# Kernel optimization log

Measured on AMD Instinct MI355X. Metric: run time of the kernel, lower is better.

The kernel has to match this reference:

```python
import jax, jax.numpy as jnp
import numpy as np

# EEACSF hyperparameters (module defaults)
CUTOFF = 5.2
ANG_CUTOFF = 3.5
RADIAL_ETA = 16.0
ANGULAR_ETA = 8.0
RDIV = 16          # radial_dist_divisions
ADIV = 4           # angular_dist_divisions
ZETA = 32.0
SECTIONS = 4       # angle_sections
R_START = 0.8
A_START = 0.8
N_SPECIES = 87     # size of periodic-table / valence table

N_ATOMS = 20000
N_EDGES = 640000       # radial edges
N_ANG_EDGES = 160000   # angular-graph edges
N_PAIRS = 560000       # angle pairs


def setup_inputs() -> dict:
    key = jax.random.key(0)
    ks = jax.random.split(key, 12)
    species = jax.random.randint(ks[0], (N_ATOMS,), 0, N_SPECIES)
    # radial graph: distances in (R_START, CUTOFF)
    distances = R_START + (CUTOFF - R_START) * jax.random.uniform(ks[1], (N_EDGES,), jnp.float32)
    switch = jax.random.uniform(ks[2], (N_EDGES,), jnp.float32)
    edge_src = jax.random.randint(ks[3], (N_EDGES,), 0, N_ATOMS)
    edge_dst = jax.random.randint(ks[4], (N_EDGES,), 0, N_ATOMS)
    # angular graph
    ang_angles = np.pi * jax.random.uniform(ks[5], (N_PAIRS,), jnp.float32)
    ang_distances = A_START + (ANG_CUTOFF - A_START) * jax.random.uniform(ks[6], (N_ANG_EDGES,), jnp.float32)
    ang_switch = jax.random.uniform(ks[7], (N_ANG_EDGES,), jnp.float32)
    ang_edge_dst = jax.random.randint(ks[8], (N_ANG_EDGES,), 0, N_ATOMS)
    angle_src = jax.random.randint(ks[9], (N_PAIRS,), 0, N_ANG_EDGES)
    angle_dst = jax.random.randint(ks[10], (N_PAIRS,), 0, N_ANG_EDGES)
    central_atom = jax.random.randint(ks[11], (N_PAIRS,), 0, N_ATOMS)
    # valence structure table (stands in for the preprocessed VALENCE_STRUCTURE constant)
    valence_table = jax.random.uniform(jax.random.fold_in(key, 99), (N_SPECIES, 4), jnp.float32)
    return {
        "species": species, "distances": distances, "switch": switch,
        "edge_src": edge_src, "edge_dst": edge_dst,
        "ang_angles": ang_angles, "ang_distances": ang_distances,
        "ang_switch": ang_switch, "ang_edge_dst": ang_edge_dst,
        "angle_src": angle_src, "angle_dst": angle_dst,
        "central_atom": central_atom, "valence_table": valence_table,
    }


def reference(species, distances, switch, edge_src, edge_dst,
              ang_angles, ang_distances, ang_switch, ang_edge_dst,
              angle_src, angle_dst, central_atom, valence_table):
    n_atoms = species.shape[0]
    valence = valence_table[species]                                  # [N,4]

    # ---- radial AEV ----
    shiftR = jnp.asarray(np.linspace(R_START, CUTOFF, RDIV + 1)[None, :-1], distances.dtype)
    x2 = RADIAL_ETA * (distances[:, None] - shiftR) ** 2              # [E,16]
    radial_terms = 0.25 * jnp.exp(-x2) * switch[:, None]              # [E,16]
    radial_aev = jax.ops.segment_sum(
        radial_terms[:, :, None] * valence[edge_dst, None, :],        # [E,16,4]
        edge_src, num_segments=n_atoms,
    ).reshape(n_atoms, -1)                                            # [N,64]

    # ---- angular AEV ----
    d12 = 0.5 * (ang_distances[angle_src] + ang_distances[angle_dst])[:, None]  # [P,1]
    angle_start = np.pi / (2 * SECTIONS)
    shiftZ = jnp.asarray((np.linspace(0, np.pi, SECTIONS + 1) + angle_start)[None, :-1], ang_distances.dtype)
    shiftA = jnp.asarray(np.linspace(A_START, ANG_CUTOFF, ADIV + 1)[None, :-1], ang_distances.dtype)
    factor1 = (0.5 + 0.5 * jnp.cos(ang_angles[:, None] - shiftZ)) ** ZETA       # [P,4]
    factor2 = jnp.exp(-ANGULAR_ETA * (d12 - shiftA) ** 2)                       # [P,4]
    angular_terms = (factor1[:, None, :] * factor2[:, :, None]).reshape(-1, SECTIONS * ADIV)
    angular_terms = angular_terms * 2 * (ang_switch[angle_src] * ang_switch[angle_dst])[:, None]  # [P,16]

    valence_dst = valence[ang_edge_dst]                               # [E2,4]
    vp = valence_dst[angle_src] + valence_dst[angle_dst]              # [P,4]
    vm = valence_dst[angle_src] * valence_dst[angle_dst]              # [P,4]
    valence_ang = (vp[:, :, None] * vm[:, None, :]).reshape(-1, 16)   # [P,16]

    angular_aev = jax.ops.segment_sum(
        angular_terms[:, :, None] * valence_ang[:, None, :],          # [P,16,16]
        central_atom, num_segments=n_atoms,
    ).reshape(n_atoms, -1)                                            # [N,256]

    onehot = jax.nn.one_hot(species, N_SPECIES, dtype=distances.dtype)  # [N,87]
    return jnp.concatenate((onehot, radial_aev, angular_aev), axis=-1)  # [N,407]
```

## Files before the change

### kernel.cpp

```cpp
#include <hip/hip_runtime.h>
#include <hip/hip_fp16.h>
#include <math.h>

#define NCOLS   407
#define RAD_OFF 87
#define ANG_OFF 151
#define T1      3072
#define KPT     (T1 / 256)
#define WB      32
#define MAXBKT  640
#define CAPF    1792
#define C2      (CAPF / 256)


typedef __attribute__((ext_vector_type(8))) _Float16 f16x8;
typedef __attribute__((ext_vector_type(4))) float    f32x4;

static __device__ inline unsigned pack2(float a, float b) {
    __half2 h = __floats2half2_rn(a, b);
    return *reinterpret_cast<unsigned*>(&h);
}
static __device__ inline float2 unpack2(unsigned u) {
    __half2 h = *reinterpret_cast<__half2*>(&u);
    return __half22float2(h);
}

__global__ __launch_bounds__(256) void zc_kernel(int* __restrict__ cursors) {
    int t = threadIdx.x;
    for (int i = t; i < 2 * MAXBKT; i += 256) cursors[i] = 0;
}

__global__ __launch_bounds__(256) void pass1_kernel(
    const float* __restrict__ dist, const float* __restrict__ sw,
    const int* __restrict__ esrc, const int* __restrict__ edst,
    const float* __restrict__ ang_angles,
    const float* __restrict__ ang_dist, const float* __restrict__ ang_sw,
    const int* __restrict__ ang_edge_dst,
    const int* __restrict__ psrc, const int* __restrict__ pdst,
    const int* __restrict__ central,
    const int* __restrict__ species, const float4* __restrict__ valence,
    uint4* __restrict__ edata,
    int* __restrict__ cur_rad, int* __restrict__ cur_ang,
    uint4* __restrict__ arr_rad, uint4* __restrict__ arr_ang,
    int n_edges, int n_pairs, int n_ang_edges,
    int nbkt, int nbe, int nt_rad)
{
    __shared__ uint4 buf[T1];
    __shared__ int   lh[MAXBKT];
    __shared__ int   gb[MAXBKT];
    __shared__ int   wtot[4];

    int bid = blockIdx.x;
    int t = threadIdx.x;

    if (bid < nbe) {
        int i = bid * 2560 + t;
        #pragma unroll
        for (int k = 0; k < 10; ++k, i += 256) {
            if (i < n_ang_edges) {
                float4 v = valence[species[ang_edge_dst[i]]];
                uint4 r;
                r.x = __float_as_uint(ang_dist[i]);
                r.y = __float_as_uint(ang_sw[i]);
                r.z = pack2(v.x, v.y);
                r.w = pack2(v.z, v.w);
                edata[i] = r;
            }
        }
        return;
    }

    int sbid = bid - nbe;
    int is_ang = sbid >= nt_rad;
    const int* key = is_ang ? central : esrc;
    int* cursor = is_ang ? cur_ang : cur_rad;
    int n   = is_ang ? n_pairs : n_edges;
    int off = (is_ang ? sbid - nt_rad : sbid) * T1;
    int cnt = min(T1, n - off);
    uint4* arr = is_ang ? arr_ang : arr_rad;

    for (int b = t; b < nbkt; b += 256) lh[b] = 0;
    __syncthreads();

    int meta[KPT];
    #pragma unroll
    for (int k = 0; k < KPT; ++k) {
        int i = off + k * 256 + t;
        meta[k] = -1;
        if (i < n) {
            int atom = key[i];
            int r = atomicAdd(&lh[atom >> 5], 1);
            meta[k] = (atom << 12) | r;
        }
    }
    __syncthreads();

    {
        int w = t >> 6, lane = t & 63;
        int W4  = (nbkt + 3) >> 2;
        int wlo = w * W4;
        int whi = min(wlo + W4, nbkt);
        int b0 = wlo + lane * 3;
        int c0 = (b0     < whi) ? lh[b0]     : 0;
        int c1 = (b0 + 1 < whi) ? lh[b0 + 1] : 0;
        int c2 = (b0 + 2 < whi) ? lh[b0 + 2] : 0;
        int lsum = c0 + c1 + c2;
        int s = lsum;
        #pragma unroll
        for (int o = 1; o < 64; o <<= 1) {
            int u = __shfl_up(s, o, 64);
            if (lane >= o) s += u;
        }
        int excl = s - lsum;
        if (c0) gb[b0]     = b0       * CAPF + atomicAdd(&cursor[b0],     c0);
        if (c1) gb[b0 + 1] = (b0 + 1) * CAPF + atomicAdd(&cursor[b0 + 1], c1);
        if (c2) gb[b0 + 2] = (b0 + 2) * CAPF + atomicAdd(&cursor[b0 + 2], c2);
        if (b0     < whi) lh[b0]     = excl;
        if (b0 + 1 < whi) lh[b0 + 1] = excl + c0;
        if (b0 + 2 < whi) lh[b0 + 2] = excl + c0 + c1;
        if (lane == 63) wtot[w] = s;
        __syncthreads();
        int wbase = 0;
        for (int ww = 0; ww < w; ++ww) wbase += wtot[ww];
        if (wbase) {
            if (b0     < whi) lh[b0]     += wbase;
            if (b0 + 1 < whi) lh[b0 + 1] += wbase;
            if (b0 + 2 < whi) lh[b0 + 2] += wbase;
        }
        __syncthreads();
    }

    #pragma unroll
    for (int k = 0; k < KPT; ++k) {
        if (meta[k] < 0) continue;
        int i = off + k * 256 + t;
        int atom = meta[k] >> 12, r = meta[k] & 4095;
        int b = atom >> 5;
        uint4 rec;
        if (!is_ang) {
            float d  = dist[i];
            float ps = 0.25f * sw[i];
            float4 v = valence[species[edst[i]]];
            rec.x = __float_as_uint(d);
            rec.y = pack2(ps * v.x, ps * v.y);
            rec.z = pack2(ps * v.z, ps * v.w);
            rec.w = (unsigned)atom;
        } else {
            rec.x = (unsigned)psrc[i];
            rec.y = (unsigned)pdst[i];
            rec.z = __float_as_uint(ang_angles[i]);
            rec.w = (unsigned)atom;
        }
        buf[lh[b] + r] = rec;
    }
    __syncthreads();

    #pragma unroll
    for (int k = 0; k < KPT; ++k) {
        int j = k * 256 + t;
        if (j < cnt) {
            uint4 r = buf[j];
            int b = (int)(r.w >> 5);
            int gpos = gb[b] + (j - lh[b]);
            if (gpos < (b + 1) * CAPF) arr[gpos] = r;
        }
    }
}

__global__ __launch_bounds__(256) void pass2B_kernel(
    const uint4* __restrict__ arr_rad, const uint4* __restrict__ arr_ang,
    const uint4* __restrict__ edata,
    const int* __restrict__ cur_rad, const int* __restrict__ cur_ang,
    const int* __restrict__ species,
    float* __restrict__ out, int nbkt, int n_atoms)
{
    __shared__ uint4 buf[CAPF];
    __shared__ unsigned short ord[CAPF];
    __shared__ int lh[WB];
    __shared__ int sA[WB + 1];
    __shared__ uint4 stg[4][256];

    int bid = blockIdx.x;
    int t = threadIdx.x;
    int g = bid >= nbkt;
    int b = g ? bid - nbkt : bid;
    int lo  = b * CAPF;
    int cnt = min(g ? cur_ang[b] : cur_rad[b], CAPF);
    const uint4* arr = g ? arr_ang : arr_rad;
    int loA = b << 5;

    if (t < WB) lh[t] = 0;
    __syncthreads();
    int myar[C2];
    #pragma unroll
    for (int c = 0; c < C2; ++c) {
        int j = c * 256 + t;
        myar[c] = -1;
        if (j < cnt) {
            uint4 r = arr[lo + j];
            buf[j] = r;
            int a = (int)r.w - loA;
            if ((unsigned)a < WB) {
                int rk = atomicAdd(&lh[a], 1);
                myar[c] = (a << 12) | rk;
            }
        }
    }
    __syncthreads();
    if (t < 64) {
        int v = (t < WB) ? lh[t] : 0;
        int s = v;
        #pragma unroll
        for (int o = 1; o < WB; o <<= 1) {
            int u = __shfl_up(s, o, 64);
            if (t >= o) s += u;
        }
        if (t < WB) sA[t + 1] = s;
        if (t == 0) sA[0] = 0;
    }
    __syncthreads();
    #pragma unroll
    for (int c = 0; c < C2; ++c) {
        if (myar[c] >= 0) {
            int j = c * 256 + t;
            ord[sA[myar[c] >> 12] + (myar[c] & 4095)] = (unsigned short)j;
        }
    }
    __syncthreads();

    int w    = t >> 6;
    int lane = t & 63;
    int m  = lane & 15;
    int g4 = lane >> 4;

    if (g) {
        const _Float16* hl = (const _Float16*)stg[w];
        int aw0 = w * 8;
        int R0 = sA[aw0], R1 = sA[aw0 + 8];
        int cur = aw0;
        f32x4 acc = {0.f, 0.f, 0.f, 0.f};

        for (int base = R0; base < R1; base += 64) {
            int idx = base + lane;
            unsigned q[16];
            if (idx < R1) {
                uint4 pr = buf[ord[idx]];
                int e1 = (int)pr.x;
                int e2 = (int)pr.y;
                float ang = __uint_as_float(pr.z);
                uint4 r1 = edata[e1];
                uint4 r2 = edata[e2];
                float d12 = 0.5f * (__uint_as_float(r1.x) + __uint_as_float(r2.x));
                float swp = 2.0f * __uint_as_float(r1.y) * __uint_as_float(r2.y);
                float2 v1a = unpack2(r1.z), v1b = unpack2(r1.w);
                float2 v2a = unpack2(r2.z), v2b = unpack2(r2.w);
                float vp[4] = {v1a.x + v2a.x, v1a.y + v2a.y, v1b.x + v2b.x, v1b.y + v2b.y};
                float vm[4] = {v1a.x * v2a.x, v1a.y * v2a.y, v1b.x * v2b.x, v1b.y * v2b.y};

                float sa, ca;
                __sincosf(ang, &sa, &ca);
                const float czv[4] = { 0.92387953f,  0.38268343f, -0.38268343f, -0.92387953f };
                const float szv[4] = { 0.38268343f,  0.92387953f,  0.92387953f,  0.38268343f };
                float f1v[4];
                #pragma unroll
                for (int z = 0; z < 4; ++z) {
                    float y = 0.5f + 0.5f * (ca * czv[z] + sa * szv[z]);
                    float y2 = y * y, y4 = y2 * y2, y8 = y4 * y4, y16 = y8 * y8;
                    f1v[z] = y16 * y16;
                }
                float f2sv[4];
                #pragma unroll
                for (int aa = 0; aa < 4; ++aa) {
                    float x = d12 - (0.8f + 0.675f * (float)aa);
                    f2sv[aa] = swp * __expf(-8.0f * x * x);
                }
                #pragma unroll
                for (int aa = 0; aa < 4; ++aa) {
                    q[aa * 2 + 0] = pack2(f2sv[aa] * f1v[0], f2sv[aa] * f1v[1]);
                    q[aa * 2 + 1] = pack2(f2sv[aa] * f1v[2], f2sv[aa] * f1v[3]);
                }
                #pragma unroll
                for (int i2 = 0; i2 < 4; ++i2) {
                    q[8 + i2 * 2 + 0] = pack2(vp[i2] * vm[0], vp[i2] * vm[1]);
                    q[8 + i2 * 2 + 1] = pack2(vp[i2] * vm[2], vp[i2] * vm[3]);
                }
            } else {
                #pragma unroll
                for (int k = 0; k < 16; ++k) q[k] = 0u;
            }
            stg[w][lane * 4 + 0] = make_uint4(q[0],  q[1],  q[2],  q[3]);
            stg[w][lane * 4 + 1] = make_uint4(q[4],  q[5],  q[6],  q[7]);
            stg[w][lane * 4 + 2] = make_uint4(q[8],  q[9],  q[10], q[11]);
            stg[w][lane * 4 + 3] = make_uint4(q[12], q[13], q[14], q[15]);
            asm volatile("s_waitcnt lgkmcnt(0)" ::: "memory");

            #pragma unroll
            for (int c = 0; c < 2; ++c) {
                int cbase = base + c * 32;
                if (cbase >= R1) break;
                while (cur < aw0 + 8) {
                    int abeg = sA[cur], aend = sA[cur + 1];
                    int lo_r = max(abeg, cbase) - cbase;
                    int hi_r = min(aend, cbase + 32) - cbase;
                    if (hi_r > lo_r) {
                        f16x8 wf, uf;
                        #pragma unroll
                        for (int i = 0; i < 8; ++i) {
                            int rr  = (g4 << 3) + i;
                            int row = c * 32 + rr;
                            bool live = (rr >= lo_r && rr < hi_r);
                            wf[i] = live ? hl[row * 32 + m] : (_Float16)0.0f;
                            uf[i] = hl[row * 32 + 16 + m];
                        }
                        acc = __builtin_amdgcn_mfma_f32_16x16x32_f16(wf, uf, acc, 0, 0, 0);
                    }
                    if (aend <= cbase + 32) {
                        int atom = loA + cur;
                        if (atom < n_atoms) {
                            float* orow = out + (size_t)atom * NCOLS + ANG_OFF;
                            #pragma unroll
                            for (int r = 0; r < 4; ++r)
                                orow[(g4 * 4 + r) * 16 + m] = acc[r];
                        }
                        acc = (f32x4){0.f, 0.f, 0.f, 0.f};
                        ++cur;
                    } else {
                        break;
                    }
                }
            }
            asm volatile("s_waitcnt lgkmcnt(0)" ::: "memory");
        }
        while (cur < aw0 + 8) {
            int atom = loA + cur;
            if (atom < n_atoms) {
                float* orow = out + (size_t)atom * NCOLS + ANG_OFF;
                #pragma unroll
                for (int r = 0; r < 4; ++r)
                    orow[(g4 * 4 + r) * 16 + m] = 0.0f;
            }
            ++cur;
        }
        return;
    }

    const _Float16* hl = (const _Float16*)buf;
    const float*    fl = (const float*)buf;
    float shiftm = 0.8f + 0.275f * (float)m;
    for (int ai = 0; ai < 8; ++ai) {
        int a = w * 8 + ai;
        int atom = loA + a;
        if (atom >= n_atoms) break;
        int beg = sA[a], end = sA[a + 1];
        f32x4 acc = {0.f, 0.f, 0.f, 0.f};

        for (int base = beg; base < end; base += 64) {
            int cnt2 = min(64, end - base);
            {
                f16x8 wf, uf;
                #pragma unroll
                for (int i = 0; i < 8; ++i) {
                    int k = (g4 << 3) + i;
                    int live = (k < cnt2);
                    int o = live ? (int)ord[base + k] : 0;
                    float d = fl[o * 4];
                    float x = d - shiftm;
                    float e = __expf(-16.0f * x * x);
                    wf[i] = live ? (_Float16)e : (_Float16)0.0f;
                    uf[i] = (live && m < 4) ? hl[o * 8 + 2 + m] : (_Float16)0.0f;
                }
                acc = __builtin_amdgcn_mfma_f32_16x16x32_f16(wf, uf, acc, 0, 0, 0);
            }
            if (cnt2 > 32) {
                f16x8 wf, uf;
                #pragma unroll
                for (int i = 0; i < 8; ++i) {
                    int k = 32 + (g4 << 3) + i;
                    int live = (k < cnt2);
                    int o = live ? (int)ord[base + k] : 0;
                    float d = fl[o * 4];
                    float x = d - shiftm;
                    float e = __expf(-16.0f * x * x);
                    wf[i] = live ? (_Float16)e : (_Float16)0.0f;
                    uf[i] = (live && m < 4) ? hl[o * 8 + 2 + m] : (_Float16)0.0f;
                }
                acc = __builtin_amdgcn_mfma_f32_16x16x32_f16(wf, uf, acc, 0, 0, 0);
            }
        }
        if (m < 4) {
            size_t rowbase = (size_t)atom * NCOLS;
            #pragma unroll
            for (int r = 0; r < 4; ++r)
                out[rowbase + RAD_OFF + (g4 * 4 + r) * 4 + m] = acc[r];
        }
    }

    for (int idx2 = t; idx2 < WB * 87; idx2 += 256) {
        int a = idx2 / 87, c = idx2 - a * 87;
        int atom = loA + a;
        if (atom < n_atoms)
            out[(size_t)atom * NCOLS + c] = (c == species[atom]) ? 1.0f : 0.0f;
    }
}

extern "C" void kernel_launch(void* const* d_in, const int* in_sizes, int n_in,
                              void* d_out, int out_size, void* d_ws, size_t ws_size,
                              hipStream_t stream) {
    const int*   species      = (const int*)  d_in[0];
    const float* distances    = (const float*)d_in[1];
    const float* switch_      = (const float*)d_in[2];
    const int*   edge_src     = (const int*)  d_in[3];
    const int*   edge_dst     = (const int*)  d_in[4];
    const float* ang_angles   = (const float*)d_in[5];
    const float* ang_dist     = (const float*)d_in[6];
    const float* ang_switch   = (const float*)d_in[7];
    const int*   ang_edge_dst = (const int*)  d_in[8];
    const int*   angle_src    = (const int*)  d_in[9];
    const int*   angle_dst    = (const int*)  d_in[10];
    const int*   central_atom = (const int*)  d_in[11];
    const float4* valence     = (const float4*)d_in[12];

    float* out = (float*)d_out;

    const int n_atoms     = in_sizes[0];
    const int n_edges     = in_sizes[1];
    const int n_ang_edges = in_sizes[6];
    const int n_pairs     = in_sizes[5];

    const int nbkt   = (n_atoms + WB - 1) / WB;
    const int nt_rad = (n_edges + T1 - 1) / T1;
    const int nt_ang = (n_pairs + T1 - 1) / T1;
    const int nbe    = (n_ang_edges + 2559) / 2560;

    char* ws = (char*)d_ws;
    size_t off = 0;
    auto alloc = [&](size_t bytes) -> void* {
        void* p = ws + off;
        off = (off + bytes + 15) & ~(size_t)15;
        return p;
    };
    uint4* arr_rad = (uint4*)alloc((size_t)nbkt * CAPF * 16);
    uint4* arr_ang = (uint4*)alloc((size_t)nbkt * CAPF * 16);
    uint4* edata   = (uint4*)alloc((size_t)n_ang_edges * 16);
    int*   cursors = (int*)  alloc((size_t)2 * MAXBKT * sizeof(int));
    int* cur_rad = cursors;
    int* cur_ang = cursors + MAXBKT;

    zc_kernel<<<1, 256, 0, stream>>>(cursors);

    pass1_kernel<<<nbe + nt_rad + nt_ang, 256, 0, stream>>>(
        distances, switch_, edge_src, edge_dst,
        ang_angles, ang_dist, ang_switch, ang_edge_dst,
        angle_src, angle_dst, central_atom,
        species, valence, edata,
        cur_rad, cur_ang, arr_rad, arr_ang,
        n_edges, n_pairs, n_ang_edges, nbkt, nbe, nt_rad);

    pass2B_kernel<<<2 * nbkt, 256, 0, stream>>>(
        arr_rad, arr_ang, edata, cur_rad, cur_ang, species, out, nbkt, n_atoms);
}
```

Measured before the change: 79.31 us.

## Replace atomic bucket cursors with deterministic two-pass tile histogram scan

Before, each pass1 tile reserved space in fixed-capacity bucket slots through global atomic cursors. Now a separate histogram pass counts keys per tile and bucket. A transposed scan plus a bucket-level scan then give exact, compact global offsets, and pass1 scatters into densely packed arrays with no atomics and no capacity clipping. This removes global atomic contention and the padded CAPF-sized arrays, but adds extra launches and a second read of the key arrays. The tile size is also shrunk.

```diff
diff --git a/kernel.cpp b/kernel.cpp
--- a/kernel.cpp
+++ b/kernel.cpp
@@ -5,7 +5,7 @@
 #define NCOLS   407
 #define RAD_OFF 87
 #define ANG_OFF 151
-#define T1      3072
+#define T1      2816
 #define KPT     (T1 / 256)
 #define WB      32
 #define MAXBKT  640
@@ -25,31 +25,17 @@
     return __half22float2(h);
 }
 
-__global__ __launch_bounds__(256) void zc_kernel(int* __restrict__ cursors) {
-    int t = threadIdx.x;
-    for (int i = t; i < 2 * MAXBKT; i += 256) cursors[i] = 0;
-}
-
-__global__ __launch_bounds__(256) void pass1_kernel(
-    const float* __restrict__ dist, const float* __restrict__ sw,
-    const int* __restrict__ esrc, const int* __restrict__ edst,
-    const float* __restrict__ ang_angles,
-    const float* __restrict__ ang_dist, const float* __restrict__ ang_sw,
-    const int* __restrict__ ang_edge_dst,
-    const int* __restrict__ psrc, const int* __restrict__ pdst,
-    const int* __restrict__ central,
-    const int* __restrict__ species, const float4* __restrict__ valence,
-    uint4* __restrict__ edata,
-    int* __restrict__ cur_rad, int* __restrict__ cur_ang,
-    uint4* __restrict__ arr_rad, uint4* __restrict__ arr_ang,
-    int n_edges, int n_pairs, int n_ang_edges,
-    int nbkt, int nbe, int nt_rad)
-{
-    __shared__ uint4 buf[T1];
-    __shared__ int   lh[MAXBKT];
-    __shared__ int   gb[MAXBKT];
-    __shared__ int   wtot[4];
-
+__global__ __launch_bounds__(256) void pass0_kernel(const int* __restrict__ esrc,
+                                                    const int* __restrict__ central,
+                                                    const float* __restrict__ ang_dist,
+                                                    const float* __restrict__ ang_sw,
+                                                    const int* __restrict__ ang_edge_dst,
+                                                    const int* __restrict__ species,
+                                                    const float4* __restrict__ valence,
+                                                    int* __restrict__ tileHistT,
+                                                    uint4* __restrict__ edata,
+                                                    int n_edges, int n_pairs, int n_ang_edges,
+                                                    int nbkt, int nbe, int nt_rad, int nt_ang) {
     int bid = blockIdx.x;
     int t = threadIdx.x;
 
@@ -70,16 +56,105 @@
         return;
     }
 
+    __shared__ int lh[MAXBKT];
     int sbid = bid - nbe;
     int is_ang = sbid >= nt_rad;
+    int tile = is_ang ? sbid - nt_rad : sbid;
     const int* key = is_ang ? central : esrc;
-    int* cursor = is_ang ? cur_ang : cur_rad;
+    int n = is_ang ? n_pairs : n_edges;
+    int off = tile * T1;
+    for (int b = t; b < nbkt; b += 256) lh[b] = 0;
+    __syncthreads();
+    #pragma unroll
+    for (int k = 0; k < KPT; ++k) {
+        int i = off + k * 256 + t;
+        if (i < n) atomicAdd(&lh[key[i] >> 5], 1);
+    }
+    __syncthreads();
+    int* base = tileHistT + (is_ang ? (size_t)nbkt * nt_rad : 0);
+    int ntg = is_ang ? nt_ang : nt_rad;
+    for (int b = t; b < nbkt; b += 256) base[(size_t)b * ntg + tile] = lh[b];
+}
+
+__global__ __launch_bounds__(256) void scanT_kernel(int* __restrict__ tileHistT,
+                                                    int* __restrict__ bktTotals,
+                                                    int nt_rad, int nt_ang, int nbkt) {
+    int wid  = blockIdx.x * 4 + (threadIdx.x >> 6);
+    int lane = threadIdx.x & 63;
+    if (wid >= 2 * nbkt) return;
+    int g = wid >= nbkt;
+    int b = g ? wid - nbkt : wid;
+    int ntg = g ? nt_ang : nt_rad;
+    int* row = tileHistT + (g ? (size_t)nbkt * nt_rad : 0) + (size_t)b * ntg;
+    int run = 0;
+    for (int k0 = 0; k0 < ntg; k0 += 64) {
+        int k = k0 + lane;
+        int v = (k < ntg) ? row[k] : 0;
+        int s = v;
+        #pragma unroll
+        for (int o = 1; o < 64; o <<= 1) {
+            int u = __shfl_up(s, o, 64);
+            if (lane >= o) s += u;
+        }
+        if (k < ntg) row[k] = run + s - v;
+        run += __shfl(s, 63, 64);
+    }
+    if (lane == 0) bktTotals[g * MAXBKT + b] = run;
+}
+
+__global__ __launch_bounds__(1024) void scanB_kernel(const int* __restrict__ bktTotals,
+                                                     int* __restrict__ bktBase, int nbkt) {
+    int g = blockIdx.x;
+    const int* tot = bktTotals + g * MAXBKT;
+    int* bb = bktBase + g * (MAXBKT + 1);
+    __shared__ int part[1024];
+    int t = threadIdx.x;
+    int v = (t < nbkt) ? tot[t] : 0;
+    part[t] = v;
+    __syncthreads();
+    for (int o = 1; o < 1024; o <<= 1) {
+        int u = (t >= o) ? part[t - o] : 0;
+        __syncthreads();
+        part[t] += u;
+        __syncthreads();
+    }
+    if (t < nbkt) bb[t] = part[t] - v;
+    if (t == nbkt - 1) bb[nbkt] = part[t];
+}
+
+__global__ __launch_bounds__(256) void pass1_kernel(
+    const float* __restrict__ dist, const float* __restrict__ sw,
+    const int* __restrict__ esrc, const int* __restrict__ edst,
+    const float* __restrict__ ang_angles,
+    const int* __restrict__ psrc, const int* __restrict__ pdst,
+    const int* __restrict__ central,
+    const int* __restrict__ species, const float4* __restrict__ valence,
+    const int* __restrict__ tileHistT, const int* __restrict__ bktBase,
+    uint4* __restrict__ arr_rad, uint4* __restrict__ arr_ang,
+    int n_edges, int n_pairs, int nbkt, int nt_rad, int nt_ang)
+{
+    __shared__ uint4 buf[T1];
+    __shared__ int   lh[MAXBKT];
+    __shared__ int   gb[MAXBKT];
+    __shared__ int   wtot[4];
+
+    int bid = blockIdx.x;
+    int t = threadIdx.x;
+    int is_ang = bid >= nt_rad;
+    int tile = is_ang ? bid - nt_rad : bid;
+    const int* key = is_ang ? central : esrc;
     int n   = is_ang ? n_pairs : n_edges;
-    int off = (is_ang ? sbid - nt_rad : sbid) * T1;
+    int off = tile * T1;
     int cnt = min(T1, n - off);
     uint4* arr = is_ang ? arr_ang : arr_rad;
-
-    for (int b = t; b < nbkt; b += 256) lh[b] = 0;
+    const int* throwT = tileHistT + (is_ang ? (size_t)nbkt * nt_rad : 0) + tile;
+    int ntg = is_ang ? nt_ang : nt_rad;
+    const int* bb = bktBase + is_ang * (MAXBKT + 1);
+
+    for (int b = t; b < nbkt; b += 256) {
+        lh[b] = 0;
+        gb[b] = bb[b] + throwT[(size_t)b * ntg];
+    }
     __syncthreads();
 
     int meta[KPT];
@@ -112,9 +187,6 @@
             if (lane >= o) s += u;
         }
         int excl = s - lsum;
-        if (c0) gb[b0]     = b0       * CAPF + atomicAdd(&cursor[b0],     c0);
-        if (c1) gb[b0 + 1] = (b0 + 1) * CAPF + atomicAdd(&cursor[b0 + 1], c1);
-        if (c2) gb[b0 + 2] = (b0 + 2) * CAPF + atomicAdd(&cursor[b0 + 2], c2);
         if (b0     < whi) lh[b0]     = excl;
         if (b0 + 1 < whi) lh[b0 + 1] = excl + c0;
         if (b0 + 2 < whi) lh[b0 + 2] = excl + c0 + c1;
@@ -161,8 +233,7 @@
         if (j < cnt) {
             uint4 r = buf[j];
             int b = (int)(r.w >> 5);
-            int gpos = gb[b] + (j - lh[b]);
-            if (gpos < (b + 1) * CAPF) arr[gpos] = r;
+            arr[gb[b] + (j - lh[b])] = r;
         }
     }
 }
@@ -170,7 +241,7 @@
 __global__ __launch_bounds__(256) void pass2B_kernel(
     const uint4* __restrict__ arr_rad, const uint4* __restrict__ arr_ang,
     const uint4* __restrict__ edata,
-    const int* __restrict__ cur_rad, const int* __restrict__ cur_ang,
+    const int* __restrict__ bktBase,
     const int* __restrict__ species,
     float* __restrict__ out, int nbkt, int n_atoms)
 {
@@ -184,8 +255,9 @@
     int t = threadIdx.x;
     int g = bid >= nbkt;
     int b = g ? bid - nbkt : bid;
-    int lo  = b * CAPF;
-    int cnt = min(g ? cur_ang[b] : cur_rad[b], CAPF);
+    const int* bb = bktBase + g * (MAXBKT + 1);
+    int lo  = bb[b];
+    int cnt = min(bb[b + 1] - lo, CAPF);
     const uint4* arr = g ? arr_ang : arr_rad;
     int loA = b << 5;
 
@@ -439,23 +511,29 @@
         off = (off + bytes + 15) & ~(size_t)15;
         return p;
     };
-    uint4* arr_rad = (uint4*)alloc((size_t)nbkt * CAPF * 16);
-    uint4* arr_ang = (uint4*)alloc((size_t)nbkt * CAPF * 16);
-    uint4* edata   = (uint4*)alloc((size_t)n_ang_edges * 16);
-    int*   cursors = (int*)  alloc((size_t)2 * MAXBKT * sizeof(int));
-    int* cur_rad = cursors;
-    int* cur_ang = cursors + MAXBKT;
-
-    zc_kernel<<<1, 256, 0, stream>>>(cursors);
-
-    pass1_kernel<<<nbe + nt_rad + nt_ang, 256, 0, stream>>>(
+    uint4* arr_rad   = (uint4*)alloc((size_t)n_edges * 16);
+    uint4* arr_ang   = (uint4*)alloc((size_t)n_pairs * 16);
+    uint4* edata     = (uint4*)alloc((size_t)n_ang_edges * 16);
+    int*   tileHistT = (int*)  alloc((size_t)nbkt * (nt_rad + nt_ang) * 4);
+    int*   bktTotals = (int*)  alloc((size_t)2 * MAXBKT * sizeof(int));
+    int*   bktBase   = (int*)  alloc((size_t)2 * (MAXBKT + 1) * sizeof(int));
+
+    pass0_kernel<<<nbe + nt_rad + nt_ang, 256, 0, stream>>>(
+        edge_src, central_atom, ang_dist, ang_switch, ang_edge_dst,
+        species, valence, tileHistT, edata,
+        n_edges, n_pairs, n_ang_edges, nbkt, nbe, nt_rad, nt_ang);
+
+    scanT_kernel<<<(2 * nbkt + 3) / 4, 256, 0, stream>>>(
+        tileHistT, bktTotals, nt_rad, nt_ang, nbkt);
+
+    scanB_kernel<<<2, 1024, 0, stream>>>(bktTotals, bktBase, nbkt);
+
+    pass1_kernel<<<nt_rad + nt_ang, 256, 0, stream>>>(
         distances, switch_, edge_src, edge_dst,
-        ang_angles, ang_dist, ang_switch, ang_edge_dst,
-        angle_src, angle_dst, central_atom,
-        species, valence, edata,
-        cur_rad, cur_ang, arr_rad, arr_ang,
-        n_edges, n_pairs, n_ang_edges, nbkt, nbe, nt_rad);
+        ang_angles, angle_src, angle_dst, central_atom,
+        species, valence, tileHistT, bktBase,
+        arr_rad, arr_ang, n_edges, n_pairs, nbkt, nt_rad, nt_ang);
 
     pass2B_kernel<<<2 * nbkt, 256, 0, stream>>>(
-        arr_rad, arr_ang, edata, cur_rad, cur_ang, species, out, nbkt, n_atoms);
-}
+        arr_rad, arr_ang, edata, bktBase, species, out, nbkt, n_atoms);
+}
```

After: 79.40 us (median of 2 runs). No clear change (+0.1%).
